# Optimization experiments

Hardware: AMD Instinct MI355X
Metric: run time of the kernel (lower is better)

The kernel has to match this reference:

```python
import jax, jax.numpy as jnp
import numpy as np

EPS = 1e-5
NUM_HEADS = 8
BLOCK_SIZE = 8


def _ln(x, w, b):
    mu = jnp.mean(x, axis=-1, keepdims=True)
    var = jnp.mean((x - mu) ** 2, axis=-1, keepdims=True)
    return (x - mu) * jax.lax.rsqrt(var + EPS) * w + b


def _mha(x, wqkv, bqkv, wo, bo, allowed):
    # x: [b,t,d]; wqkv: [3d,d]; allowed: [t,t] bool (True = attend)
    b, t, d = x.shape
    h, hd = NUM_HEADS, d // NUM_HEADS
    qkv = x @ wqkv.T + bqkv
    q, k, v = jnp.split(qkv, 3, axis=-1)
    q = q.reshape(b, t, h, hd)
    k = k.reshape(b, t, h, hd)
    v = v.reshape(b, t, h, hd)
    scores = jnp.einsum('bihd,bjhd->bhij', q, k) / np.sqrt(hd).astype(x.dtype)
    scores = jnp.where(allowed[None, None], scores, -jnp.inf)
    attn = jax.nn.softmax(scores, axis=-1)
    out = jnp.einsum('bhij,bjhd->bihd', attn, v).reshape(b, t, d)
    return out @ wo.T + bo


def setup_inputs() -> dict:
    key = jax.random.key(0)
    ks = jax.random.split(key, 20)
    B, T, D, FF, L, MAXT = 64, 512, 256, 512, 4, 512
    s = 0.02
    return {
        'latents': jax.random.normal(ks[0], (B, T, D), dtype=jnp.float32),
        'move_ids': jax.random.randint(ks[1], (B, T), 0, 20480),
        'mask': jax.random.randint(ks[2], (B, T), 0, 2).astype(bool),
        'positional': s * jax.random.normal(ks[3], (1, MAXT, D), dtype=jnp.float32),
        'embed_from': s * jax.random.normal(ks[4], (64, D), dtype=jnp.float32),
        'embed_to': s * jax.random.normal(ks[5], (64, D), dtype=jnp.float32),
        'embed_promo': s * jax.random.normal(ks[6], (5, D), dtype=jnp.float32),
        'in_proj_w': s * jax.random.normal(ks[7], (L, 3 * D, D), dtype=jnp.float32),
        'in_proj_b': jnp.zeros((L, 3 * D), dtype=jnp.float32),
        'out_w': s * jax.random.normal(ks[8], (L, D, D), dtype=jnp.float32),
        'out_b': jnp.zeros((L, D), dtype=jnp.float32),
        'fc1_w': s * jax.random.normal(ks[9], (L, FF, D), dtype=jnp.float32),
        'fc1_b': jnp.zeros((L, FF), dtype=jnp.float32),
        'fc2_w': s * jax.random.normal(ks[10], (L, D, FF), dtype=jnp.float32),
        'fc2_b': jnp.zeros((L, D), dtype=jnp.float32),
        'norm_w': jnp.ones((D,), dtype=jnp.float32),
        'norm_b': jnp.zeros((D,), dtype=jnp.float32),
    }


def reference(latents, move_ids, mask, positional, embed_from, embed_to,
              embed_promo, in_proj_w, in_proj_b, out_w, out_b,
              fc1_w, fc1_b, fc2_w, fc2_b, norm_w, norm_b):
    b, t, d = latents.shape
    # move-id decomposition: promo/from/to embedding sum
    promo = move_ids // 4096
    rem = move_ids % 4096
    frm = rem // 64
    to = rem % 64
    x = latents + positional[:, :t, :] + embed_from[frm] + embed_to[to] + embed_promo[promo]
    # block-causal mask: token i may attend j iff block(j) <= block(i)
    bidx = jnp.arange(t) // BLOCK_SIZE
    allowed = bidx[None, :] <= bidx[:, None]
    n_layers = in_proj_w.shape[0]
    for l in range(n_layers):
        # NOTE: the single LayerNorm (norm_w, norm_b) is shared everywhere,
        # exactly as in the original module.
        x = x + _mha(_ln(x, norm_w, norm_b), in_proj_w[l], in_proj_b[l],
                     out_w[l], out_b[l], allowed)
        h1 = jax.nn.relu(_ln(x, norm_w, norm_b) @ fc1_w[l].T + fc1_b[l])
        x = x + h1 @ fc2_w[l].T + fc2_b[l]
    x = _ln(x, norm_w, norm_b)
    return jnp.where(mask[..., None], x, latents)
```

## Files before the change

### kernel.cpp

```cpp
#include <hip/hip_runtime.h>
#include <math.h>

#define Bv  64
#define Tv  512
#define Dv  256
#define FFv 512
#define Lv  4
#define BTv (Bv*Tv)
#define EPSv 1e-5f
#define QSC 0.25509402f

typedef __attribute__((ext_vector_type(8))) short short8;
typedef __attribute__((ext_vector_type(4))) float f32x4;
typedef unsigned short us;

#if __has_builtin(__builtin_amdgcn_exp2f)
#define EXP2(x) __builtin_amdgcn_exp2f(x)
#else
#define EXP2(x) exp2f(x)
#endif

__device__ __forceinline__ us f2bf(float f) {
    unsigned r;
    asm("v_cvt_pk_bf16_f32 %0, %1, 0" : "=v"(r) : "v"(f));
    return (us)r;
}
__device__ __forceinline__ unsigned pk2(float a, float b) {
    unsigned r;
    asm("v_cvt_pk_bf16_f32 %0, %1, %2" : "=v"(r) : "v"(a), "v"(b));
    return r;
}
__device__ __forceinline__ float wave_sum(float v) {
#pragma unroll
    for (int o = 32; o > 0; o >>= 1) v += __shfl_xor(v, o);
    return v;
}

__global__ __launch_bounds__(256) void cvtall_kernel(
    const float* __restrict__ qw, const float* __restrict__ ow,
    const float* __restrict__ f1, const float* __restrict__ f2,
    const float* __restrict__ qb,
    us* __restrict__ wq, us* __restrict__ wo, us* __restrict__ w1,
    us* __restrict__ w2, float* __restrict__ sb)
{
    int blk = blockIdx.x, tid = threadIdx.x;
    if (blk < 2048) {
        const float* s; us* d; int i; float sc = 1.0f;
        if (blk < 768)       { i = blk*256 + tid;        s = qw; d = wq;
                               sc = (((i >> 6) % 768) < 256) ? QSC : 1.0f; }
        else if (blk < 1024) { i = (blk-768)*256 + tid;  s = ow; d = wo; }
        else if (blk < 1536) { i = (blk-1024)*256 + tid; s = f1; d = w1; }
        else                 { i = (blk-1536)*256 + tid; s = f2; d = w2; }
        float4 v = ((const float4*)s)[i];
        uint2 o;
        o.x = pk2(v.x*sc, v.y*sc);
        o.y = pk2(v.z*sc, v.w*sc);
        ((uint2*)d)[i] = o;
    } else {
        int i = (blk-2048)*256 + tid;
        sb[i] = qb[i] * (((i % 768) < 256) ? QSC : 1.0f);
    }
}

__global__ __launch_bounds__(256) void embed_ln_kernel(
    const float* __restrict__ lat, const int* __restrict__ mids,
    const float* __restrict__ pos, const float* __restrict__ ef,
    const float* __restrict__ et,  const float* __restrict__ ep,
    const float* __restrict__ nw,  const float* __restrict__ nb,
    float* __restrict__ x, us* __restrict__ xn)
{
    int wv = threadIdx.x >> 6, lane = threadIdx.x & 63;
    size_t row = (size_t)blockIdx.x * 4 + wv;
    int t  = (int)(row & (Tv - 1));
    int id = mids[row];
    int promo = id >> 12;
    int rem   = id & 4095;
    int frm   = rem >> 6;
    int to    = rem & 63;
    float4 v  = ((const float4*)(lat + row*Dv))[lane];
    float4 pv = ((const float4*)(pos + (size_t)t*Dv))[lane];
    float4 fv = ((const float4*)(ef + (size_t)frm*Dv))[lane];
    float4 tv = ((const float4*)(et + (size_t)to*Dv))[lane];
    float4 ev = ((const float4*)(ep + (size_t)promo*Dv))[lane];
    v.x += pv.x + fv.x + tv.x + ev.x;
    v.y += pv.y + fv.y + tv.y + ev.y;
    v.z += pv.z + fv.z + tv.z + ev.z;
    v.w += pv.w + fv.w + tv.w + ev.w;
    ((float4*)(x + row*Dv))[lane] = v;
    float mu = wave_sum(v.x + v.y + v.z + v.w) * (1.0f/Dv);
    float dx = v.x-mu, dy = v.y-mu, dz = v.z-mu, dw = v.w-mu;
    float var = wave_sum(dx*dx + dy*dy + dz*dz + dw*dw) * (1.0f/Dv);
    float inv = rsqrtf(var + EPSv);
    float4 w4 = ((const float4*)nw)[lane];
    float4 b4 = ((const float4*)nb)[lane];
    uint2 o;
    o.x = pk2(dx*inv*w4.x + b4.x, dy*inv*w4.y + b4.y);
    o.y = pk2(dz*inv*w4.z + b4.z, dw*inv*w4.w + b4.w);
    ((uint2*)(xn + row*Dv))[lane] = o;
}

__global__ __launch_bounds__(256) void final_kernel(
    const float* __restrict__ x, const float* __restrict__ lat,
    const int* __restrict__ mask, const float* __restrict__ w,
    const float* __restrict__ b, float* __restrict__ out)
{
    int wv = threadIdx.x >> 6, lane = threadIdx.x & 63;
    size_t row = (size_t)blockIdx.x * 4 + wv;
    float4 v = ((const float4*)(x + row*Dv))[lane];
    float mu = wave_sum(v.x + v.y + v.z + v.w) * (1.0f/Dv);
    float dx = v.x-mu, dy = v.y-mu, dz = v.z-mu, dw = v.w-mu;
    float var = wave_sum(dx*dx + dy*dy + dz*dz + dw*dw) * (1.0f/Dv);
    float inv = rsqrtf(var + EPSv);
    float4 w4 = ((const float4*)w)[lane];
    float4 b4 = ((const float4*)b)[lane];
    float4 o;
    o.x = dx*inv*w4.x + b4.x;
    o.y = dy*inv*w4.y + b4.y;
    o.z = dz*inv*w4.z + b4.z;
    o.w = dw*inv*w4.w + b4.w;
    if (!mask[row]) o = ((const float4*)(lat + row*Dv))[lane];
    ((float4*)(out + row*Dv))[lane] = o;
}

template<int RELU>
__global__ __launch_bounds__(256) void mm_kernel(
    const us* __restrict__ A, const us* __restrict__ B,
    const float* __restrict__ bias, us* __restrict__ C,
    int M, int N, int K)
{
    __shared__ us As[128*64];
    __shared__ us Bs[128*64];
    int tid  = threadIdx.x;
    int lane = tid & 63;
    int wu   = __builtin_amdgcn_readfirstlane(tid >> 6);
    int m0 = blockIdx.x * 128, n0 = blockIdx.y * 128;
    int wm = wu & 1, wn = wu >> 1;
    f32x4 acc[4][4] = {};
    int srow = lane >> 3;
    int sg   = (lane & 7) ^ srow;
    const us* Ag = A + (size_t)m0 * K + sg*8;
    const us* Bg = B + (size_t)n0 * K + sg*8;
    int cc = lane & 15, q4 = lane >> 4;
    for (int k0 = 0; k0 < K; k0 += 64) {
        __syncthreads();
#pragma unroll
        for (int p = 0; p < 4; p++) {
            int row = wu*32 + p*8;
            __builtin_amdgcn_global_load_lds(
                (const __attribute__((address_space(1))) unsigned int*)(Ag + (size_t)(row + srow)*K + k0),
                (__attribute__((address_space(3))) unsigned int*)(As + row*64),
                16, 0, 0);
            __builtin_amdgcn_global_load_lds(
                (const __attribute__((address_space(1))) unsigned int*)(Bg + (size_t)(row + srow)*K + k0),
                (__attribute__((address_space(3))) unsigned int*)(Bs + row*64),
                16, 0, 0);
        }
        __syncthreads();
#pragma unroll
        for (int h = 0; h < 2; h++) {
            int pg = ((h*4 + q4) ^ (cc & 7)) * 8;
            short8 av[4], bv[4];
#pragma unroll
            for (int i = 0; i < 4; i++)
                av[i] = *(const short8*)(As + (wm*64 + i*16 + cc)*64 + pg);
#pragma unroll
            for (int j = 0; j < 4; j++)
                bv[j] = *(const short8*)(Bs + (wn*64 + j*16 + cc)*64 + pg);
#pragma unroll
            for (int i = 0; i < 4; i++)
#pragma unroll
                for (int j = 0; j < 4; j++)
                    acc[i][j] = __builtin_amdgcn_mfma_f32_16x16x32_bf16(av[i], bv[j], acc[i][j], 0, 0, 0);
        }
    }
#pragma unroll
    for (int j = 0; j < 4; j++) {
        int n = n0 + wn*64 + j*16 + cc;
        float bj = bias[n];
#pragma unroll
        for (int i = 0; i < 4; i++) {
#pragma unroll
            for (int r = 0; r < 4; r++) {
                int m = m0 + wm*64 + i*16 + q4*4 + r;
                float v = acc[i][j][r] + bj;
                if (RELU) v = fmaxf(v, 0.f);
                C[(size_t)m * N + n] = f2bf(v);
            }
        }
    }
}

__global__ __launch_bounds__(512) void mmfuse_kernel(
    const us* __restrict__ A, const us* __restrict__ B,
    const float* __restrict__ bias, float* __restrict__ x,
    us* __restrict__ xn, const float* __restrict__ nw,
    const float* __restrict__ nb, int M, int K)
{
    __shared__ us As[2][128*64];
    __shared__ us Bs[2][256*64];
    __shared__ float red[128][4][2];
    __shared__ float mus[128], rss[128];
    int tid  = threadIdx.x;
    int lane = tid & 63;
    int wu   = __builtin_amdgcn_readfirstlane(tid >> 6);
    int m0 = blockIdx.x * 128;
    int wm = wu & 1, wn = wu >> 1;
    f32x4 acc[4][4] = {};
    int srow = lane >> 3;
    int sg   = (lane & 7) ^ srow;
    const us* Ag = A + (size_t)m0 * K + sg*8;
    const us* Bg = B + sg*8;
    int cc = lane & 15, q4 = lane >> 4;

#define STG(kk, bb) { \
    _Pragma("unroll") \
    for (int p = 0; p < 2; p++) { \
        int row = wu*16 + p*8; \
        __builtin_amdgcn_global_load_lds( \
            (const __attribute__((address_space(1))) unsigned int*)(Ag + (size_t)(row + srow)*K + (kk)), \
            (__attribute__((address_space(3))) unsigned int*)(&As[bb][row*64]), \
            16, 0, 0); \
    } \
    _Pragma("unroll") \
    for (int p = 0; p < 4; p++) { \
        int row = wu*32 + p*8; \
        __builtin_amdgcn_global_load_lds( \
            (const __attribute__((address_space(1))) unsigned int*)(Bg + (size_t)(row + srow)*K + (kk)), \
            (__attribute__((address_space(3))) unsigned int*)(&Bs[bb][row*64]), \
            16, 0, 0); \
    } }

    STG(0, 0);
    __syncthreads();
    int nk = K >> 6;
    int cur = 0;
    for (int t = 0; t < nk; t++) {
        if (t + 1 < nk) {
            if (cur) STG((t+1)*64, 0) else STG((t+1)*64, 1)
        }
#pragma unroll
        for (int h = 0; h < 2; h++) {
            int pg = ((h*4 + q4) ^ (cc & 7)) * 8;
            short8 av[4], bv[4];
#pragma unroll
            for (int i = 0; i < 4; i++)
                av[i] = *(const short8*)(&As[cur][(wm*64 + i*16 + cc)*64 + pg]);
#pragma unroll
            for (int j = 0; j < 4; j++)
                bv[j] = *(const short8*)(&Bs[cur][(wn*64 + j*16 + cc)*64 + pg]);
#pragma unroll
            for (int i = 0; i < 4; i++)
#pragma unroll
                for (int j = 0; j < 4; j++)
                    acc[i][j] = __builtin_amdgcn_mfma_f32_16x16x32_bf16(av[i], bv[j], acc[i][j], 0, 0, 0);
        }
        __syncthreads();
        cur ^= 1;
    }
#undef STG

    float bb4[4], nwv[4], nbv[4];
#pragma unroll
    for (int j = 0; j < 4; j++) {
        int n = wn*64 + j*16 + cc;
        bb4[j] = bias[n]; nwv[j] = nw[n]; nbv[j] = nb[n];
    }
#pragma unroll
    for (int i = 0; i < 4; i++) {
        float s[4] = {0.f,0.f,0.f,0.f}, sq[4] = {0.f,0.f,0.f,0.f};
#pragma unroll
        for (int j = 0; j < 4; j++) {
#pragma unroll
            for (int r = 0; r < 4; r++) {
                int ml = wm*64 + i*16 + q4*4 + r;
                size_t off = (size_t)(m0 + ml) * Dv + wn*64 + j*16 + cc;
                float v = acc[i][j][r] + bb4[j] + x[off];
                acc[i][j][r] = v;
                x[off] = v;
                s[r] += v; sq[r] += v*v;
            }
        }
#pragma unroll
        for (int r = 0; r < 4; r++) {
#pragma unroll
            for (int o = 1; o < 16; o <<= 1) {
                s[r]  += __shfl_xor(s[r],  o);
                sq[r] += __shfl_xor(sq[r], o);
            }
        }
        if (cc == 0) {
#pragma unroll
            for (int r = 0; r < 4; r++) {
                red[wm*64 + i*16 + q4*4 + r][wn][0] = s[r];
                red[wm*64 + i*16 + q4*4 + r][wn][1] = sq[r];
            }
        }
    }
    __syncthreads();
    if (tid < 128) {
        float ts = red[tid][0][0] + red[tid][1][0] + red[tid][2][0] + red[tid][3][0];
        float tq = red[tid][0][1] + red[tid][1][1] + red[tid][2][1] + red[tid][3][1];
        float mu = ts * (1.0f/Dv);
        float var = tq * (1.0f/Dv) - mu*mu;
        mus[tid] = mu;
        rss[tid] = rsqrtf(var + EPSv);
    }
    __syncthreads();
#pragma unroll
    for (int i = 0; i < 4; i++) {
#pragma unroll
        for (int r = 0; r < 4; r++) {
            int ml = wm*64 + i*16 + q4*4 + r;
            float mu = mus[ml], rv = rss[ml];
#pragma unroll
            for (int j = 0; j < 4; j++) {
                size_t off = (size_t)(m0 + ml) * Dv + wn*64 + j*16 + cc;
                xn[off] = f2bf((acc[i][j][r] - mu)*rv*nwv[j] + nbv[j]);
            }
        }
    }
}

__global__ __launch_bounds__(256) void attn_kernel(
    const us* __restrict__ qkv, us* __restrict__ ao)
{
    int blk = blockIdx.x;
    int b  = blk & 63;
    int h  = (blk >> 6) & 7;
    int qt = blk >> 9;
    int i0 = qt << 6;
    int tid = threadIdx.x;
    int lane = tid & 63;
    int wu = tid >> 6;

    __shared__ us Ks[2][64][40];
    __shared__ us Vt[2][32][72];
    __shared__ us Ps[4][16][72];
    __shared__ float Ls[4][16];

    size_t rowbase = (size_t)b * Tv;
    int c = lane & 15, q4 = lane >> 4;

    short8 qfrag = *(const short8*)(qkv + (rowbase + i0 + wu*16 + c)*768 + h*32 + q4*8);

    int skey = tid >> 2, sdc = (tid & 3) << 3;
    int vkey = tid & 63, vg = tid >> 6;
    const us* kgp = qkv + (rowbase + skey)*768 + 256 + h*32 + sdc;
    const us* vgp = qkv + (rowbase + vkey)*768 + 512 + h*32 + vg*8;

    f32x4 oacc[2] = {};
    float lsum = 0.f;
    int ntiles = qt + 1;

    short8 kreg = *(const short8*)(kgp);
    short8 vreg = *(const short8*)(vgp);
    *(short8*)&Ks[0][skey][sdc] = kreg;
#pragma unroll
    for (int j = 0; j < 8; j++) Vt[0][vg*8 + j][vkey] = vreg[j];
    if (ntiles > 1) {
        kreg = *(const short8*)(kgp + 64*768);
        vreg = *(const short8*)(vgp + 64*768);
    }
    __syncthreads();

    for (int kt = 0; kt < ntiles; kt++) {
        int cur = kt & 1;
        if (kt + 1 < ntiles) {
            *(short8*)&Ks[cur^1][skey][sdc] = kreg;
#pragma unroll
            for (int j = 0; j < 8; j++) Vt[cur^1][vg*8 + j][vkey] = vreg[j];
        }
        if (kt + 2 < ntiles) {
            kreg = *(const short8*)(kgp + (size_t)(kt+2)*64*768);
            vreg = *(const short8*)(vgp + (size_t)(kt+2)*64*768);
        }

        f32x4 st[4];
#pragma unroll
        for (int jt = 0; jt < 4; jt++) {
            short8 kf = *(const short8*)&Ks[cur][jt*16 + c][q4*8];
            st[jt] = __builtin_amdgcn_mfma_f32_16x16x32_bf16(kf, qfrag, (f32x4){0.f,0.f,0.f,0.f}, 0, 0, 0);
        }
        bool diag = (kt == ntiles - 1);
#pragma unroll
        for (int jt = 0; jt < 4; jt++) {
            float msk = (!diag || (2*jt + (q4 >> 1) <= 2*wu + (c >> 3))) ? 1.f : 0.f;
            float p0 = EXP2(st[jt][0]) * msk;
            float p1 = EXP2(st[jt][1]) * msk;
            float p2 = EXP2(st[jt][2]) * msk;
            float p3 = EXP2(st[jt][3]) * msk;
            lsum += p0 + p1 + p2 + p3;
            uint2 w2; w2.x = pk2(p0, p1); w2.y = pk2(p2, p3);
            *(uint2*)&Ps[wu][c][jt*16 + q4*4] = w2;
        }
#pragma unroll
        for (int kk = 0; kk < 2; kk++) {
            short8 pf = *(const short8*)&Ps[wu][c][kk*32 + q4*8];
#pragma unroll
            for (int dt = 0; dt < 2; dt++) {
                short8 vf = *(const short8*)&Vt[cur][dt*16 + c][kk*32 + q4*8];
                oacc[dt] = __builtin_amdgcn_mfma_f32_16x16x32_bf16(pf, vf, oacc[dt], 0, 0, 0);
            }
        }
        __syncthreads();
    }

    float l = lsum;
    l += __shfl_xor(l, 16);
    l += __shfl_xor(l, 32);
    if (q4 == 0) Ls[wu][c] = 1.0f / l;
    float4 lv4 = *(const float4*)&Ls[wu][q4*4];
#pragma unroll
    for (int dt = 0; dt < 2; dt++) {
#pragma unroll
        for (int r = 0; r < 4; r++) {
            float li = (r == 0) ? lv4.x : (r == 1) ? lv4.y : (r == 2) ? lv4.z : lv4.w;
            ao[(rowbase + i0 + wu*16 + q4*4 + r)*256 + h*32 + dt*16 + c] = f2bf(oacc[dt][r] * li);
        }
    }
}

extern "C" void kernel_launch(void* const* d_in, const int* in_sizes, int n_in,
                              void* d_out, int out_size, void* d_ws, size_t ws_size,
                              hipStream_t stream)
{
    const float* latents    = (const float*)d_in[0];
    const int*   move_ids   = (const int*)  d_in[1];
    const int*   mask       = (const int*)  d_in[2];
    const float* positional = (const float*)d_in[3];
    const float* embed_from = (const float*)d_in[4];
    const float* embed_to   = (const float*)d_in[5];
    const float* embed_promo= (const float*)d_in[6];
    const float* in_proj_w  = (const float*)d_in[7];
    const float* in_proj_b  = (const float*)d_in[8];
    const float* out_w      = (const float*)d_in[9];
    const float* out_b      = (const float*)d_in[10];
    const float* fc1_w      = (const float*)d_in[11];
    const float* fc1_b      = (const float*)d_in[12];
    const float* fc2_w      = (const float*)d_in[13];
    const float* fc2_b      = (const float*)d_in[14];
    const float* norm_w     = (const float*)d_in[15];
    const float* norm_b     = (const float*)d_in[16];
    float* out = (float*)d_out;

    float* x   = (float*)d_ws;
    float* sb  = x + (size_t)BTv * Dv;
    us* xn  = (us*)(sb + Lv*768);
    us* qkv = xn + (size_t)BTv * Dv;
    us* ao  = qkv + (size_t)BTv * 768;
    us* h1  = ao + (size_t)BTv * Dv;
    us* wq  = h1 + (size_t)BTv * FFv;
    us* wo  = wq + (size_t)Lv * 768 * Dv;
    us* w1  = wo + (size_t)Lv * Dv * Dv;
    us* w2  = w1 + (size_t)Lv * FFv * Dv;

    cvtall_kernel<<<2060, 256, 0, stream>>>(in_proj_w, out_w, fc1_w, fc2_w,
                                            in_proj_b, wq, wo, w1, w2, sb);

    embed_ln_kernel<<<BTv/4, 256, 0, stream>>>(latents, move_ids, positional,
        embed_from, embed_to, embed_promo, norm_w, norm_b, x, xn);

    for (int l = 0; l < Lv; l++) {
        mm_kernel<0><<<dim3(BTv/128, 768/128), 256, 0, stream>>>(
            xn, wq + (size_t)l*768*Dv, sb + l*768, qkv, BTv, 768, Dv);
        attn_kernel<<<Bv*8*(Tv/64), 256, 0, stream>>>(qkv, ao);
        mmfuse_kernel<<<BTv/128, 512, 0, stream>>>(
            ao, wo + (size_t)l*Dv*Dv, out_b + l*Dv, x, xn, norm_w, norm_b,
            BTv, Dv);
        mm_kernel<1><<<dim3(BTv/128, FFv/128), 256, 0, stream>>>(
            xn, w1 + (size_t)l*FFv*Dv, fc1_b + l*FFv, h1, BTv, FFv, Dv);
        mmfuse_kernel<<<BTv/128, 512, 0, stream>>>(
            h1, w2 + (size_t)l*Dv*FFv, fc2_b + l*Dv, x, xn, norm_w, norm_b,
            BTv, FFv);
    }
    final_kernel<<<BTv/4, 256, 0, stream>>>(x, latents, mask, norm_w, norm_b, out);
}
```

Baseline: 626.4 us.

## Double-buffer plain GEMM and prefetch two stages ahead with vmcnt waits

```diff
diff --git a/kernel.cpp b/kernel.cpp
--- a/kernel.cpp
+++ b/kernel.cpp
@@ -19,6 +19,8 @@
 #else
 #define EXP2(x) exp2f(x)
 #endif
+
+#define WAITV(n) asm volatile("s_waitcnt vmcnt(" #n ")" ::: "memory")
 
 __device__ __forceinline__ us f2bf(float f) {
     unsigned r;
@@ -128,8 +130,8 @@
     const float* __restrict__ bias, us* __restrict__ C,
     int M, int N, int K)
 {
-    __shared__ us As[128*64];
-    __shared__ us Bs[128*64];
+    __shared__ us As[2][128*64];
+    __shared__ us Bs[2][128*64];
     int tid  = threadIdx.x;
     int lane = tid & 63;
     int wu   = __builtin_amdgcn_readfirstlane(tid >> 6);
@@ -141,38 +143,52 @@
     const us* Ag = A + (size_t)m0 * K + sg*8;
     const us* Bg = B + (size_t)n0 * K + sg*8;
     int cc = lane & 15, q4 = lane >> 4;
-    for (int k0 = 0; k0 < K; k0 += 64) {
-        __syncthreads();
-#pragma unroll
-        for (int p = 0; p < 4; p++) {
-            int row = wu*32 + p*8;
-            __builtin_amdgcn_global_load_lds(
-                (const __attribute__((address_space(1))) unsigned int*)(Ag + (size_t)(row + srow)*K + k0),
-                (__attribute__((address_space(3))) unsigned int*)(As + row*64),
-                16, 0, 0);
-            __builtin_amdgcn_global_load_lds(
-                (const __attribute__((address_space(1))) unsigned int*)(Bg + (size_t)(row + srow)*K + k0),
-                (__attribute__((address_space(3))) unsigned int*)(Bs + row*64),
-                16, 0, 0);
-        }
-        __syncthreads();
+
+#define STG(kk, bb) { \
+    _Pragma("unroll") \
+    for (int p = 0; p < 4; p++) { \
+        int row = wu*32 + p*8; \
+        __builtin_amdgcn_global_load_lds( \
+            (const __attribute__((address_space(1))) unsigned int*)(Ag + (size_t)(row + srow)*K + (kk)), \
+            (__attribute__((address_space(3))) unsigned int*)(&As[bb][row*64]), \
+            16, 0, 0); \
+        __builtin_amdgcn_global_load_lds( \
+            (const __attribute__((address_space(1))) unsigned int*)(Bg + (size_t)(row + srow)*K + (kk)), \
+            (__attribute__((address_space(3))) unsigned int*)(&Bs[bb][row*64]), \
+            16, 0, 0); \
+    } }
+
+    int nk = K >> 6;
+    STG(0, 0);
+    if (nk > 1) STG(64, 1);
+    int cur = 0;
+    for (int t = 0; t < nk; t++) {
+        if (t < nk - 1) { WAITV(8); } else { WAITV(0); }
+        __builtin_amdgcn_s_barrier();
+        __builtin_amdgcn_sched_barrier(0);
 #pragma unroll
         for (int h = 0; h < 2; h++) {
             int pg = ((h*4 + q4) ^ (cc & 7)) * 8;
             short8 av[4], bv[4];
 #pragma unroll
             for (int i = 0; i < 4; i++)
-                av[i] = *(const short8*)(As + (wm*64 + i*16 + cc)*64 + pg);
+                av[i] = *(const short8*)(&As[cur][(wm*64 + i*16 + cc)*64 + pg]);
 #pragma unroll
             for (int j = 0; j < 4; j++)
-                bv[j] = *(const short8*)(Bs + (wn*64 + j*16 + cc)*64 + pg);
+                bv[j] = *(const short8*)(&Bs[cur][(wn*64 + j*16 + cc)*64 + pg]);
 #pragma unroll
             for (int i = 0; i < 4; i++)
 #pragma unroll
                 for (int j = 0; j < 4; j++)
                     acc[i][j] = __builtin_amdgcn_mfma_f32_16x16x32_bf16(av[i], bv[j], acc[i][j], 0, 0, 0);
         }
-    }
+        __builtin_amdgcn_sched_barrier(0);
+        __builtin_amdgcn_s_barrier();
+        __builtin_amdgcn_sched_barrier(0);
+        if (t + 2 < nk) STG((t+2)*64, cur);
+        cur ^= 1;
+    }
+#undef STG
 #pragma unroll
     for (int j = 0; j < 4; j++) {
         int n = n0 + wn*64 + j*16 + cc;
@@ -230,14 +246,14 @@
             16, 0, 0); \
     } }
 
+    int nk = K >> 6;
     STG(0, 0);
-    __syncthreads();
-    int nk = K >> 6;
+    if (nk > 1) STG(64, 1);
     int cur = 0;
     for (int t = 0; t < nk; t++) {
-        if (t + 1 < nk) {
-            if (cur) STG((t+1)*64, 0) else STG((t+1)*64, 1)
-        }
+        if (t < nk - 1) { WAITV(6); } else { WAITV(0); }
+        __builtin_amdgcn_s_barrier();
+        __builtin_amdgcn_sched_barrier(0);
 #pragma unroll
         for (int h = 0; h < 2; h++) {
             int pg = ((h*4 + q4) ^ (cc & 7)) * 8;
@@ -254,7 +270,10 @@
                 for (int j = 0; j < 4; j++)
                     acc[i][j] = __builtin_amdgcn_mfma_f32_16x16x32_bf16(av[i], bv[j], acc[i][j], 0, 0, 0);
         }
-        __syncthreads();
+        __builtin_amdgcn_sched_barrier(0);
+        __builtin_amdgcn_s_barrier();
+        __builtin_amdgcn_sched_barrier(0);
+        if (t + 2 < nk) STG((t+2)*64, cur);
         cur ^= 1;
     }
 #undef STG
```

Result: no change. 621.0 us (-0.9%).
